# Kernel tuning notes

Hardware: AMD Instinct MI355X
Metric: run time of the kernel (lower is better)

## Reference

```python
import jax, jax.numpy as jnp
import numpy as np

KEY_CH = 256

def _conv1x1(w, b, t):
    # 1x1 conv with BN folded: t [B,Cin,N] -> [B,Cout,N]
    return jnp.einsum('oc,bcn->bon', w, t) + b[None, :, None]

def _conv1x1_relu(w, b, t):
    return jax.nn.relu(_conv1x1(w, b, t))

def setup_inputs() -> dict:
    key = jax.random.key(0)
    ks = jax.random.split(key, 12)
    B, C, H, W = 4, 512, 128, 128
    d = {}
    d['feat'] = jax.random.normal(ks[0], (B, C, H, W), jnp.float32)
    d['prob'] = jax.random.normal(ks[1], (B, 20, H, W), jnp.float32)  # unused by forward (overwritten)
    s = 0.02
    d['wp1'] = jax.random.normal(ks[2], (KEY_CH, C), jnp.float32) * s
    d['bp1'] = jnp.zeros((KEY_CH,), jnp.float32)
    d['wp2'] = jax.random.normal(ks[3], (KEY_CH, KEY_CH), jnp.float32) * s
    d['bp2'] = jnp.zeros((KEY_CH,), jnp.float32)
    d['wo1'] = jax.random.normal(ks[4], (KEY_CH, C), jnp.float32) * s
    d['bo1'] = jnp.zeros((KEY_CH,), jnp.float32)
    d['wo2'] = jax.random.normal(ks[5], (KEY_CH, KEY_CH), jnp.float32) * s
    d['bo2'] = jnp.zeros((KEY_CH,), jnp.float32)
    d['wd'] = jax.random.normal(ks[6], (KEY_CH, C), jnp.float32) * s
    d['bd'] = jnp.zeros((KEY_CH,), jnp.float32)
    d['wu'] = jax.random.normal(ks[7], (C, KEY_CH), jnp.float32) * s
    d['bu'] = jnp.zeros((C,), jnp.float32)
    d['wout'] = jax.random.normal(ks[8], (512, 2 * C), jnp.float32) * s
    d['bout'] = jnp.zeros((512,), jnp.float32)
    return d


def reference(feat, prob, wp1, bp1, wp2, bp2, wo1, bo1, wo2, bo2, wd, bd, wu, bu, wout, bout):
    B, C, H, W = feat.shape
    x = feat.reshape(B, C, H * W)  # [B,C,N]
    # prob = upsample_bilinear(feat, (H,W)) == feat (identity resize); prob arg is dead.
    # SpatialGather (scale=1): softmax over spatial, weighted pool of features.
    pw = jax.nn.softmax(x, axis=-1)                     # [B,K,N], K == C here
    context = jnp.einsum('bkn,bcn->bck', pw, x)         # [B,C,K] proxy features
    # ObjectAttentionBlock2D
    q = _conv1x1_relu(wp2, bp2, _conv1x1_relu(wp1, bp1, x))        # [B,key,N]
    k = _conv1x1_relu(wo2, bo2, _conv1x1_relu(wo1, bo1, context))  # [B,key,K]
    v = _conv1x1_relu(wd, bd, context)                             # [B,key,K]
    sim = jnp.einsum('bdn,bdk->bnk', q, k) * (KEY_CH ** -0.5)      # [B,N,K]
    sim = jax.nn.softmax(sim, axis=-1)
    ctx = jnp.einsum('bnk,bdk->bdn', sim, v)                       # [B,key,N]
    ctx = _conv1x1_relu(wu, bu, ctx)                               # [B,C,N]
    # SpatialOCR: concat + 1x1 conv + BN + ReLU (dropout identity at eval)
    out = _conv1x1_relu(wout, bout, jnp.concatenate([ctx, x], axis=1))  # [B,out,N]
    return out.reshape(B, -1, H, W)
```

## Files before the change

kernel.cpp:

```cpp
#include <hip/hip_runtime.h>

typedef unsigned int u32;
typedef unsigned short u16;
typedef short s16x8 __attribute__((ext_vector_type(8)));
typedef float f32x4 __attribute__((ext_vector_type(4)));

__device__ __forceinline__ u16 f2bf(float f) {
  u32 u = __float_as_uint(f);
  u32 r = (u + 0x7fffu + ((u >> 16) & 1u)) >> 16;
  return (u16)r;
}

template <int MODE>
__device__ __forceinline__ uint4 pack8(const float* p, float2 st) {
  float4 f0 = *(const float4*)p;
  float4 f1 = *(const float4*)(p + 4);
  float v[8] = {f0.x, f0.y, f0.z, f0.w, f1.x, f1.y, f1.z, f1.w};
  if (MODE == 2) {
#pragma unroll
    for (int j = 0; j < 8; ++j) v[j] = __expf(v[j] - st.x) * st.y;
  }
  uint4 o;
  o.x = (u32)f2bf(v[0]) | ((u32)f2bf(v[1]) << 16);
  o.y = (u32)f2bf(v[2]) | ((u32)f2bf(v[3]) << 16);
  o.z = (u32)f2bf(v[4]) | ((u32)f2bf(v[5]) << 16);
  o.w = (u32)f2bf(v[6]) | ((u32)f2bf(v[7]) << 16);
  return o;
}

__global__ __launch_bounds__(256) void row_softmax_bf16(
    const float* __restrict__ feat, u16* __restrict__ expx) {
  const long long row = blockIdx.x;
  const float* xp = feat + row * 16384;
  const int tid = threadIdx.x, wv = tid >> 6, ln = tid & 63;
  __shared__ float red[4];
  float mx = -1e30f;
  for (int i = tid * 4; i < 16384; i += 1024) {
    float4 r = *(const float4*)(xp + i);
    mx = fmaxf(mx, fmaxf(fmaxf(r.x, r.y), fmaxf(r.z, r.w)));
  }
  for (int o = 32; o; o >>= 1) mx = fmaxf(mx, __shfl_xor(mx, o, 64));
  if (!ln) red[wv] = mx;
  __syncthreads();
  mx = fmaxf(fmaxf(red[0], red[1]), fmaxf(red[2], red[3]));
  __syncthreads();
  float s = 0.f;
  for (int i = tid * 4; i < 16384; i += 1024) {
    float4 r = *(const float4*)(xp + i);
    s += __expf(r.x - mx) + __expf(r.y - mx) + __expf(r.z - mx) + __expf(r.w - mx);
  }
  for (int o = 32; o; o >>= 1) s += __shfl_xor(s, o, 64);
  if (!ln) red[wv] = s;
  __syncthreads();
  const float inv = 1.f / (red[0] + red[1] + red[2] + red[3]);
  const float2 st = make_float2(mx, inv);
  u16* op = expx + row * 16384;
  for (int i = tid * 8; i < 16384; i += 2048) {
    uint4 o = pack8<2>(xp + i, st);
    *(uint4*)(op + i) = o;
  }
}

__global__ __launch_bounds__(256) void transpose_x(const float* __restrict__ feat,
                                                   u16* __restrict__ catT) {
  __shared__ u16 t[32][33];
  const int b = blockIdx.z;
  const int c0 = blockIdx.y << 5, n0 = blockIdx.x << 5;
  const int tx = threadIdx.x & 31, ty = threadIdx.x >> 5;
  const float* fb = feat + (long long)b * 512 * 16384;
#pragma unroll
  for (int i = 0; i < 32; i += 8)
    t[ty + i][tx] = f2bf(fb[(long long)(c0 + ty + i) * 16384 + n0 + tx]);
  __syncthreads();
  u16* ob = catT + (long long)b * 16384 * 1024 + 512;
#pragma unroll
  for (int i = 0; i < 32; i += 8)
    ob[(long long)(n0 + ty + i) * 1024 + c0 + tx] = t[tx][ty + i];
}

__global__ __launch_bounds__(256) void cvt_weights(
    const float* __restrict__ w0, const float* __restrict__ w1,
    const float* __restrict__ w2, const float* __restrict__ w3,
    const float* __restrict__ w4, const float* __restrict__ w5,
    const float* __restrict__ w6, u16* __restrict__ dst) {
  const long long i = (long long)blockIdx.x * 256 + threadIdx.x;
  const float* s;
  long long off;
  if (i < 131072) { s = w0; off = 0; }
  else if (i < 196608) { s = w1; off = 131072; }
  else if (i < 327680) { s = w2; off = 196608; }
  else if (i < 393216) { s = w3; off = 327680; }
  else if (i < 524288) { s = w4; off = 393216; }
  else if (i < 655360) { s = w5; off = 524288; }
  else { s = w6; off = 655360; }
  dst[i] = f2bf(s[i - off]);
}

template <int ACT, int BIAS, int SPLITK, int AMODE, int BMODE, int F32OUT>
__global__ __launch_bounds__(256, 2) void gemm_nt(
    const void* __restrict__ Av, long long sA, int lda,
    const void* __restrict__ Bv, long long sB, int ldb,
    void* __restrict__ C, long long sC, int ldc,
    const float* __restrict__ bias, int K, int kchunk,
    const float2* __restrict__ stats, int statsStride) {
  __shared__ __align__(16) u16 Asm_[128 * 32];
  __shared__ __align__(16) u16 Bsm_[128 * 32];
  const int tid = threadIdx.x;
  const int wv = tid >> 6;
  const int ln = tid & 63;
  const int bz = blockIdx.z;
  const int batch = SPLITK ? (bz >> 3) : bz;
  const int chunk = SPLITK ? (bz & 7) : 0;
  const long long tm = (long long)blockIdx.y << 7;
  const long long tn = (long long)blockIdx.x << 7;
  const int lrow = ln >> 2;
  const int lcol = (ln & 3) << 3;
  const int w32 = wv << 5;
  const long long ar0 = tm + w32 + lrow, ar1 = ar0 + 16;
  const long long br0 = tn + w32 + lrow, br1 = br0 + 16;
  const long long koff = (long long)chunk * kchunk + lcol;
  const u16* gau0; const u16* gau1; const float* gaf0; const float* gaf1;
  if (AMODE == 0) {
    const u16* Ab = (const u16*)Av + (long long)batch * sA + koff;
    gau0 = Ab + ar0 * lda; gau1 = Ab + ar1 * lda; gaf0 = gaf1 = nullptr;
  } else {
    const float* Ab = (const float*)Av + (long long)batch * sA + koff;
    gaf0 = Ab + ar0 * lda; gaf1 = Ab + ar1 * lda; gau0 = gau1 = nullptr;
  }
  const u16* gbu0; const u16* gbu1; const float* gbf0; const float* gbf1;
  if (BMODE == 0) {
    const u16* Bb = (const u16*)Bv + (long long)batch * sB + koff;
    gbu0 = Bb + br0 * ldb; gbu1 = Bb + br1 * ldb; gbf0 = gbf1 = nullptr;
  } else {
    const float* Bb = (const float*)Bv + (long long)batch * sB + koff;
    gbf0 = Bb + br0 * ldb; gbf1 = Bb + br1 * ldb; gbu0 = gbu1 = nullptr;
  }
  float2 stA0 = make_float2(0.f, 0.f), stA1 = stA0;
  if (AMODE == 2) {
    stA0 = stats[batch * statsStride + (int)ar0];
    stA1 = stats[batch * statsStride + (int)ar1];
  }
  u16* la0 = &Asm_[w32 * 32 + ln * 8];
  u16* la1 = la0 + 512;
  u16* lb0 = &Bsm_[w32 * 32 + ln * 8];
  u16* lb1 = lb0 + 512;
  const int fr = ln & 15;
  const int fq = ln >> 4;
  const int wm = (wv >> 1) << 6;
  const int wn = (wv & 1) << 6;
  f32x4 acc[4][4] = {};
  for (int kk = 0; kk < K; kk += 32) {
    uint4 ra0, ra1, rb0, rb1;
    if (AMODE == 0) {
      ra0 = *(const uint4*)(gau0 + kk);
      ra1 = *(const uint4*)(gau1 + kk);
    } else {
      ra0 = pack8<AMODE>(gaf0 + kk, stA0);
      ra1 = pack8<AMODE>(gaf1 + kk, stA1);
    }
    if (BMODE == 0) {
      rb0 = *(const uint4*)(gbu0 + kk);
      rb1 = *(const uint4*)(gbu1 + kk);
    } else {
      rb0 = pack8<BMODE>(gbf0 + kk, stA0);
      rb1 = pack8<BMODE>(gbf1 + kk, stA1);
    }
    __syncthreads();
    *(uint4*)la0 = ra0;
    *(uint4*)la1 = ra1;
    *(uint4*)lb0 = rb0;
    *(uint4*)lb1 = rb1;
    __syncthreads();
    s16x8 af[4], bfr[4];
#pragma unroll
    for (int i = 0; i < 4; ++i)
      af[i] = *(const s16x8*)&Asm_[(wm + i * 16 + fr) * 32 + fq * 8];
#pragma unroll
    for (int j = 0; j < 4; ++j)
      bfr[j] = *(const s16x8*)&Bsm_[(wn + j * 16 + fr) * 32 + fq * 8];
#pragma unroll
    for (int i = 0; i < 4; ++i)
#pragma unroll
      for (int j = 0; j < 4; ++j)
        acc[i][j] =
            __builtin_amdgcn_mfma_f32_16x16x32_bf16(af[i], bfr[j], acc[i][j], 0, 0, 0);
  }
#pragma unroll
  for (int i = 0; i < 4; ++i) {
    const long long gr0 = tm + wm + i * 16 + fq * 4;
#pragma unroll
    for (int j = 0; j < 4; ++j) {
      const long long gc = tn + wn + j * 16 + fr;
      float bc = 0.f;
      if (BIAS == 2) bc = bias[gc];
#pragma unroll
      for (int t = 0; t < 4; ++t) {
        float v = acc[i][j][t];
        if (BIAS == 1) v += bias[gr0 + t];
        if (BIAS == 2) v += bc;
        if (ACT) v = fmaxf(v, 0.f);
        const long long idx = (long long)batch * sC + (gr0 + t) * ldc + gc;
        if (SPLITK)
          atomicAdd((float*)C + idx, v);
        else if (F32OUT)
          ((float*)C)[idx] = v;
        else
          ((u16*)C)[idx] = f2bf(v);
      }
    }
  }
}

__global__ __launch_bounds__(256) void cvt_f32_bf16(const float* __restrict__ s,
                                                    u16* __restrict__ d) {
  const int i = blockIdx.x * 256 + threadIdx.x;
  d[i] = f2bf(s[i]);
}

__global__ __launch_bounds__(256) void softmax_p(u16* __restrict__ P) {
  const int wv = threadIdx.x >> 6, ln = threadIdx.x & 63;
  const long long row = (long long)blockIdx.x * 4 + wv;
  u16* rp = P + row * 1024;
  uint4 r = *(const uint4*)(rp + ln * 8);
  u32 w[4] = {r.x, r.y, r.z, r.w};
  float v[8];
#pragma unroll
  for (int k = 0; k < 4; ++k) {
    v[2 * k] = __uint_as_float(w[k] << 16) * 0.0625f;
    v[2 * k + 1] = __uint_as_float(w[k] & 0xffff0000u) * 0.0625f;
  }
  float m = v[0];
#pragma unroll
  for (int t = 1; t < 8; ++t) m = fmaxf(m, v[t]);
  for (int o = 32; o; o >>= 1) m = fmaxf(m, __shfl_xor(m, o, 64));
  float e[8], s = 0.f;
#pragma unroll
  for (int t = 0; t < 8; ++t) {
    e[t] = __expf(v[t] - m);
    s += e[t];
  }
  for (int o = 32; o; o >>= 1) s += __shfl_xor(s, o, 64);
  const float inv = 1.f / s;
  u32 ow[4];
#pragma unroll
  for (int k = 0; k < 4; ++k)
    ow[k] = (u32)f2bf(e[2 * k] * inv) | ((u32)f2bf(e[2 * k + 1] * inv) << 16);
  *(uint4*)(rp + ln * 8) = make_uint4(ow[0], ow[1], ow[2], ow[3]);
}

extern "C" void kernel_launch(void* const* d_in, const int* in_sizes, int n_in,
                              void* d_out, int out_size, void* d_ws, size_t ws_size,
                              hipStream_t stream) {
  const float* feat = (const float*)d_in[0];
  const float* wp1 = (const float*)d_in[2];
  const float* bp1 = (const float*)d_in[3];
  const float* wp2 = (const float*)d_in[4];
  const float* bp2 = (const float*)d_in[5];
  const float* wo1 = (const float*)d_in[6];
  const float* bo1 = (const float*)d_in[7];
  const float* wo2 = (const float*)d_in[8];
  const float* bo2 = (const float*)d_in[9];
  const float* wd = (const float*)d_in[10];
  const float* bd = (const float*)d_in[11];
  const float* wu = (const float*)d_in[12];
  const float* bu = (const float*)d_in[13];
  const float* wout = (const float*)d_in[14];
  const float* bout = (const float*)d_in[15];
  float* outp = (float*)d_out;
  char* ws = (char*)d_ws;

  u16* catT = (u16*)ws;
  u16* expx = (u16*)(ws + 134217728LL);
  u16* q1T = (u16*)(ws + 134217728LL);
  u16* ctxT = q1T;
  u16* qT = (u16*)(ws + 167772160LL);
  float* ctxF = (float*)(ws + 201326592LL);
  u16* wb = (u16*)(ws + 201326592LL);
  u16* conT = (u16*)(ws + 205520896LL);
  u16* k1hT = (u16*)(ws + 207618048LL);
  u16* kTm = (u16*)(ws + 208666624LL);
  u16* vm = (u16*)(ws + 209715200LL);
  if (ws_size < 210763776ULL) return;
  u16* wp1b = wb + 0;
  u16* wp2b = wb + 131072;
  u16* wo1b = wb + 196608;
  u16* wo2b = wb + 327680;
  u16* wdb = wb + 393216;
  u16* wub = wb + 524288;
  u16* woutb = wb + 655360;

  row_softmax_bf16<<<2048, 256, 0, stream>>>(feat, expx);
  transpose_x<<<dim3(512, 16, 4), 256, 0, stream>>>(feat, catT);
  hipMemsetAsync(ctxF, 0, 4194304, stream);
  gemm_nt<0, 0, 1, 0, 1, 0><<<dim3(4, 4, 32), 256, 0, stream>>>(
      expx, 8388608LL, 16384, feat, 8388608LL, 16384, ctxF, 262144LL, 512,
      nullptr, 2048, 2048, nullptr, 0);
  cvt_f32_bf16<<<4096, 256, 0, stream>>>(ctxF, conT);
  cvt_weights<<<4608, 256, 0, stream>>>(wp1, wp2, wo1, wo2, wd, wu, wout, wb);
  gemm_nt<1, 2, 0, 0, 0, 0><<<dim3(2, 4, 4), 256, 0, stream>>>(
      conT, 262144LL, 512, wo1b, 0LL, 512, k1hT, 131072LL, 256, bo1, 512, 0,
      nullptr, 0);
  gemm_nt<1, 2, 0, 0, 0, 0><<<dim3(2, 4, 4), 256, 0, stream>>>(
      k1hT, 131072LL, 256, wo2b, 0LL, 256, kTm, 131072LL, 256, bo2, 256, 0,
      nullptr, 0);
  gemm_nt<1, 1, 0, 0, 0, 0><<<dim3(4, 2, 4), 256, 0, stream>>>(
      wdb, 0LL, 512, conT, 262144LL, 512, vm, 131072LL, 512, bd, 512, 0,
      nullptr, 0);
  gemm_nt<1, 2, 0, 0, 0, 0><<<dim3(2, 128, 4), 256, 0, stream>>>(
      catT + 512, 16777216LL, 1024, wp1b, 0LL, 512, q1T, 4194304LL, 256, bp1,
      512, 0, nullptr, 0);
  gemm_nt<1, 2, 0, 0, 0, 0><<<dim3(2, 128, 4), 256, 0, stream>>>(
      q1T, 4194304LL, 256, wp2b, 0LL, 256, qT, 4194304LL, 256, bp2, 256, 0,
      nullptr, 0);
  gemm_nt<0, 0, 0, 0, 0, 0><<<dim3(4, 128, 4), 256, 0, stream>>>(
      qT, 4194304LL, 256, kTm, 131072LL, 256, catT, 16777216LL, 1024, nullptr,
      256, 0, nullptr, 0);
  softmax_p<<<16384, 256, 0, stream>>>(catT);
  gemm_nt<0, 0, 0, 0, 0, 0><<<dim3(2, 128, 4), 256, 0, stream>>>(
      catT, 16777216LL, 1024, vm, 131072LL, 512, ctxT, 4194304LL, 256, nullptr,
      512, 0, nullptr, 0);
  gemm_nt<1, 2, 0, 0, 0, 0><<<dim3(4, 128, 4), 256, 0, stream>>>(
      ctxT, 4194304LL, 256, wub, 0LL, 256, catT, 16777216LL, 1024, bu, 256, 0,
      nullptr, 0);
  gemm_nt<1, 1, 0, 0, 0, 1><<<dim3(128, 4, 4), 256, 0, stream>>>(
      woutb, 0LL, 1024, catT, 16777216LL, 1024, outp, 8388608LL, 16384, bout,
      1024, 0, nullptr, 0);
}
```

Before: 731.8 us.

## Use direct global-to-LDS loads for bf16 GEMMs and pre-convert x to bf16

When both GEMM operands are already bf16, tiles are now moved with global_load_lds straight into shared memory instead of passing through registers. The row-softmax kernel also writes a bf16 copy of x into the output buffer, used as scratch. The context GEMM then reads bf16 B instead of converting fp32 on the fly, which halves its B-operand traffic. The cost is an extra 64MB write in the softmax kernel, plus a dependence on the LDS address layout matching what per-lane global_load_lds writes.

New measurement: 719.3 us. About the same (-1.7%).

```diff
diff --git a/kernel.cpp b/kernel.cpp
--- a/kernel.cpp
+++ b/kernel.cpp
@@ -28,8 +28,15 @@
   return o;
 }
 
+__device__ __forceinline__ void g2l16(u16* lds, const u16* g) {
+  __builtin_amdgcn_global_load_lds(
+      (const __attribute__((address_space(1))) void*)g,
+      (__attribute__((address_space(3))) void*)lds, 16, 0, 0);
+}
+
 __global__ __launch_bounds__(256) void row_softmax_bf16(
-    const float* __restrict__ feat, u16* __restrict__ expx) {
+    const float* __restrict__ feat, u16* __restrict__ expx,
+    u16* __restrict__ xbf) {
   const long long row = blockIdx.x;
   const float* xp = feat + row * 16384;
   const int tid = threadIdx.x, wv = tid >> 6, ln = tid & 63;
@@ -55,9 +62,10 @@
   const float inv = 1.f / (red[0] + red[1] + red[2] + red[3]);
   const float2 st = make_float2(mx, inv);
   u16* op = expx + row * 16384;
+  u16* bp = xbf + row * 16384;
   for (int i = tid * 8; i < 16384; i += 2048) {
-    uint4 o = pack8<2>(xp + i, st);
-    *(uint4*)(op + i) = o;
+    *(uint4*)(op + i) = pack8<2>(xp + i, st);
+    *(uint4*)(bp + i) = pack8<0>(xp + i, st);
   }
 }
 
@@ -140,9 +148,9 @@
     stA0 = stats[batch * statsStride + (int)ar0];
     stA1 = stats[batch * statsStride + (int)ar1];
   }
-  u16* la0 = &Asm_[w32 * 32 + ln * 8];
+  u16* la0 = &Asm_[w32 * 32];
   u16* la1 = la0 + 512;
-  u16* lb0 = &Bsm_[w32 * 32 + ln * 8];
+  u16* lb0 = &Bsm_[w32 * 32];
   u16* lb1 = lb0 + 512;
   const int fr = ln & 15;
   const int fq = ln >> 4;
@@ -150,27 +158,36 @@
   const int wn = (wv & 1) << 6;
   f32x4 acc[4][4] = {};
   for (int kk = 0; kk < K; kk += 32) {
-    uint4 ra0, ra1, rb0, rb1;
-    if (AMODE == 0) {
-      ra0 = *(const uint4*)(gau0 + kk);
-      ra1 = *(const uint4*)(gau1 + kk);
+    if (AMODE == 0 && BMODE == 0) {
+      __syncthreads();
+      g2l16(la0, gau0 + kk);
+      g2l16(la1, gau1 + kk);
+      g2l16(lb0, gbu0 + kk);
+      g2l16(lb1, gbu1 + kk);
+      __syncthreads();
     } else {
-      ra0 = pack8<AMODE>(gaf0 + kk, stA0);
-      ra1 = pack8<AMODE>(gaf1 + kk, stA1);
+      uint4 ra0, ra1, rb0, rb1;
+      if (AMODE == 0) {
+        ra0 = *(const uint4*)(gau0 + kk);
+        ra1 = *(const uint4*)(gau1 + kk);
+      } else {
+        ra0 = pack8<AMODE>(gaf0 + kk, stA0);
+        ra1 = pack8<AMODE>(gaf1 + kk, stA1);
+      }
+      if (BMODE == 0) {
+        rb0 = *(const uint4*)(gbu0 + kk);
+        rb1 = *(const uint4*)(gbu1 + kk);
+      } else {
+        rb0 = pack8<BMODE>(gbf0 + kk, stA0);
+        rb1 = pack8<BMODE>(gbf1 + kk, stA1);
+      }
+      __syncthreads();
+      *(uint4*)(la0 + ln * 8) = ra0;
+      *(uint4*)(la1 + ln * 8) = ra1;
+      *(uint4*)(lb0 + ln * 8) = rb0;
+      *(uint4*)(lb1 + ln * 8) = rb1;
+      __syncthreads();
     }
-    if (BMODE == 0) {
-      rb0 = *(const uint4*)(gbu0 + kk);
-      rb1 = *(const uint4*)(gbu1 + kk);
-    } else {
-      rb0 = pack8<BMODE>(gbf0 + kk, stA0);
-      rb1 = pack8<BMODE>(gbf1 + kk, stA1);
-    }
-    __syncthreads();
-    *(uint4*)la0 = ra0;
-    *(uint4*)la1 = ra1;
-    *(uint4*)lb0 = rb0;
-    *(uint4*)lb1 = rb1;
-    __syncthreads();
     s16x8 af[4], bfr[4];
 #pragma unroll
     for (int i = 0; i < 4; ++i)
@@ -281,6 +298,7 @@
   u16* kTm = (u16*)(ws + 208666624LL);
   u16* vm = (u16*)(ws + 209715200LL);
   if (ws_size < 210763776ULL) return;
+  u16* xbf = (u16*)d_out;
   u16* wp1b = wb + 0;
   u16* wp2b = wb + 131072;
   u16* wo1b = wb + 196608;
@@ -289,11 +307,11 @@
   u16* wub = wb + 524288;
   u16* woutb = wb + 655360;
 
-  row_softmax_bf16<<<2048, 256, 0, stream>>>(feat, expx);
+  row_softmax_bf16<<<2048, 256, 0, stream>>>(feat, expx, xbf);
   transpose_x<<<dim3(512, 16, 4), 256, 0, stream>>>(feat, catT);
   hipMemsetAsync(ctxF, 0, 4194304, stream);
-  gemm_nt<0, 0, 1, 0, 1, 0><<<dim3(4, 4, 32), 256, 0, stream>>>(
-      expx, 8388608LL, 16384, feat, 8388608LL, 16384, ctxF, 262144LL, 512,
+  gemm_nt<0, 0, 1, 0, 0, 0><<<dim3(4, 4, 32), 256, 0, stream>>>(
+      expx, 8388608LL, 16384, xbf, 8388608LL, 16384, ctxF, 262144LL, 512,
       nullptr, 2048, 2048, nullptr, 0);
   cvt_f32_bf16<<<4096, 256, 0, stream>>>(ctxF, conT);
   cvt_weights<<<4608, 256, 0, stream>>>(wp1, wp2, wo1, wo2, wd, wu, wout, wb);
```
